# Kernel optimization log

Hardware: AMD Instinct MI355X
Metric: run time of the kernel (lower is better)

## Reference

```python
import jax, jax.numpy as jnp
import numpy as np

B, S = 1, 2048
HIDDEN = 2560
NH, NKV, HD = 32, 8, 128
GS = 128  # awq group size
ROPE_THETA = 1000000.0


def dequant_q4(qweight, scales, qzeros):
    """Unpack int4 AWQ weights -> dense [K, N] float weight.
    qweight: [K//8, N] int32, 8 nibbles packed along the input (K) dim.
    scales/qzeros: [K//GS, N]. w = (nibble - zero) * scale.
    """
    K8, N = qweight.shape
    shifts = jnp.arange(8, dtype=jnp.int32) * 4
    nib = (qweight[:, None, :] >> shifts[None, :, None]) & 0xF  # [K//8, 8, N]
    w = nib.reshape(K8 * 8, N).astype(scales.dtype)             # [K, N]
    z = jnp.repeat(qzeros.astype(scales.dtype), GS, axis=0)     # [K, N]
    s = jnp.repeat(scales, GS, axis=0)                          # [K, N]
    return (w - z) * s


def linear_q4(x, qw, sc, qz, bias=None):
    w = dequant_q4(qw, sc, qz)                     # [K, N]
    y = jnp.einsum('bsk,kn->bsn', x, w)
    return y + bias if bias is not None else y


def rotate_half(x):
    x1, x2 = jnp.split(x, 2, axis=-1)
    return jnp.concatenate([-x2, x1], axis=-1)


def apply_rope(q, k, cos, sin):
    # cos/sin: [B, S, HD] -> broadcast over heads at dim 2
    c = cos[:, :, None, :]
    s = sin[:, :, None, :]
    return q * c + rotate_half(q) * s, k * c + rotate_half(k) * s


def setup_inputs() -> dict:
    key = jax.random.key(0)
    ks = jax.random.split(key, 12)

    x = jax.random.normal(ks[0], (B, S, HIDDEN), dtype=jnp.float32)

    # genuine rotary embedding tables
    inv_freq = 1.0 / (ROPE_THETA ** (np.arange(0, HD, 2, dtype=np.float32) / HD))
    t = np.arange(S, dtype=np.float32)
    freqs = np.outer(t, inv_freq)                      # [S, HD/2]
    emb = np.concatenate([freqs, freqs], axis=-1)      # [S, HD]
    cos = jnp.asarray(np.cos(emb)[None], dtype=jnp.float32)  # [1, S, HD]
    sin = jnp.asarray(np.sin(emb)[None], dtype=jnp.float32)

    def mk_proj(kq, ksc, kz, K, N, group=GS):
        qw = jax.random.randint(kq, (K // 8, N), 0, 2**31 - 1, dtype=jnp.int32)
        sc = jax.random.normal(ksc, (K // group, N), dtype=jnp.float32) * 0.01
        qz = jax.random.randint(kz, (K // group, N), 0, 16, dtype=jnp.int32)
        return qw, sc, qz

    q_qweight, q_scales, q_qzeros = mk_proj(ks[1], ks[2], ks[3], HIDDEN, NH * HD)
    k_qweight, k_scales, k_qzeros = mk_proj(ks[4], ks[5], ks[6], HIDDEN, NKV * HD)
    v_qweight, v_scales, v_qzeros = mk_proj(ks[7], ks[8], ks[9], HIDDEN, NKV * HD)
    o_qweight, o_scales, o_qzeros = mk_proj(ks[10], ks[11], jax.random.fold_in(key, 99), NH * HD, HIDDEN)

    kb = jax.random.split(jax.random.fold_in(key, 7), 3)
    q_bias = jax.random.normal(kb[0], (NH * HD,), dtype=jnp.float32) * 0.02
    k_bias = jax.random.normal(kb[1], (NKV * HD,), dtype=jnp.float32) * 0.02
    v_bias = jax.random.normal(kb[2], (NKV * HD,), dtype=jnp.float32) * 0.02

    return dict(x=x, cos=cos, sin=sin,
                q_scales=q_scales, q_bias=q_bias,
                k_scales=k_scales, k_bias=k_bias,
                v_scales=v_scales, v_bias=v_bias,
                o_scales=o_scales,
                q_qweight=q_qweight, q_qzeros=q_qzeros,
                k_qweight=k_qweight, k_qzeros=k_qzeros,
                v_qweight=v_qweight, v_qzeros=v_qzeros,
                o_qweight=o_qweight, o_qzeros=o_qzeros)


def reference(x, cos, sin,
              q_scales, q_bias, k_scales, k_bias, v_scales, v_bias, o_scales,
              q_qweight, q_qzeros, k_qweight, k_qzeros,
              v_qweight, v_qzeros, o_qweight, o_qzeros):
    b, s, _ = x.shape
    xq = linear_q4(x, q_qweight, q_scales, q_qzeros, q_bias).reshape(b, s, NH, HD)
    xk = linear_q4(x, k_qweight, k_scales, k_qzeros, k_bias).reshape(b, s, NKV, HD)
    xv = linear_q4(x, v_qweight, v_scales, v_qzeros, v_bias).reshape(b, s, NKV, HD)

    xq, xk = apply_rope(xq, xk, cos, sin)

    # GQA: repeat KV heads to match query heads (prefill, start_pos=0)
    rep = NH // NKV
    xk = jnp.repeat(xk, rep, axis=2)   # [b, s, NH, HD]
    xv = jnp.repeat(xv, rep, axis=2)

    scale = 1.0 / jnp.sqrt(jnp.asarray(HD, dtype=xq.dtype))
    scores = jnp.einsum('bqhd,bkhd->bhqk', xq, xk) * scale  # [b, NH, s, s]
    causal = jnp.tril(jnp.ones((s, s), dtype=bool))
    scores = jnp.where(causal[None, None], scores, jnp.finfo(scores.dtype).min)
    attn = jax.nn.softmax(scores, axis=-1)
    out = jnp.einsum('bhqk,bkhd->bqhd', attn, xv).reshape(b, s, NH * HD)

    return linear_q4(out, o_qweight, o_scales, o_qzeros)  # [b, s, HIDDEN]
```

## Files before the change

kernel.cpp:

```cpp
#include <hip/hip_runtime.h>
#include <hip/hip_bf16.h>
#include <cstdint>

#define S_LEN 2048
#define HIDDEN 2560
#define NH 32
#define NKV 8
#define HD 128
#define GS 128

typedef __attribute__((ext_vector_type(8))) _Float16 half8v;
typedef __attribute__((ext_vector_type(2))) _Float16 half2v;
typedef __attribute__((ext_vector_type(4))) float f32x4;
typedef unsigned int uint;
typedef unsigned short ushort;

__device__ inline ushort f2h(float f) {
    _Float16 h = (_Float16)f;
    return __builtin_bit_cast(ushort, h);
}
__device__ inline float h2f(ushort u) {
    return (float)__builtin_bit_cast(_Float16, u);
}
__device__ inline uint pk2(ushort a, ushort b) { return (uint)a | ((uint)b << 16); }

__device__ __attribute__((always_inline)) inline void gl_lds16(const void* g, void* l) {
    __builtin_amdgcn_global_load_lds(
        (const __attribute__((address_space(1))) unsigned int*)g,
        (__attribute__((address_space(3))) unsigned int*)l, 16, 0, 0);
}

__global__ __launch_bounds__(320) void xcvt_kernel(
    const float* __restrict__ X, ushort* __restrict__ Xf)
{
    const int row = blockIdx.x;
    const int t   = threadIdx.x;
    const size_t base = (size_t)row * HIDDEN + t * 8;
    float4 a = *(const float4*)&X[base];
    float4 b = *(const float4*)&X[base + 4];
    uint4 hw = {pk2(f2h(a.x), f2h(a.y)), pk2(f2h(a.z), f2h(a.w)),
                pk2(f2h(b.x), f2h(b.y)), pk2(f2h(b.z), f2h(b.w))};
    *(uint4*)&Xf[base] = hw;
}

__global__ __launch_bounds__(512) void qkv5_kernel(
    const ushort* __restrict__ Xf,
    const int* __restrict__ q_qw, const float* __restrict__ q_sc,
    const int* __restrict__ q_qz, const float* __restrict__ q_b,
    const int* __restrict__ k_qw, const float* __restrict__ k_sc,
    const int* __restrict__ k_qz, const float* __restrict__ k_b,
    const int* __restrict__ v_qw, const float* __restrict__ v_sc,
    const int* __restrict__ v_qz, const float* __restrict__ v_b,
    const float* __restrict__ cosb, const float* __restrict__ sinb,
    ushort* __restrict__ Qf, ushort* __restrict__ Kf,
    ushort* __restrict__ Vrm)
{
    __shared__ __align__(16) char LDSB[65536];
    ushort* A0 = (ushort*)(LDSB);
    ushort* A1 = (ushort*)(LDSB + 16384);
    ushort* Bt = (ushort*)(LDSB + 32768);

    const int t  = threadIdx.x;
    const int w  = t >> 6;
    const int l  = t & 63;
    const int lg = l >> 4;
    const int lr = l & 15;
    const int wr = w >> 2;
    const int wc = w & 3;
    const int K  = HIDDEN;

    const int bid = blockIdx.x;
    const int swz = (bid & 7) * 48 + (bid >> 3);
    const int nblk = swz % 24;
    const int m0   = (swz / 24) * 128;

    int region, nbase, Nw;
    const int* QW; const float* SC; const int* QZ; const float* BI;
    if (nblk < 16)      { region = 0; nbase = nblk * 256;        Nw = NH * HD;
                          QW = q_qw; SC = q_sc; QZ = q_qz; BI = q_b; }
    else if (nblk < 20) { region = 1; nbase = (nblk - 16) * 256; Nw = NKV * HD;
                          QW = k_qw; SC = k_sc; QZ = k_qz; BI = k_b; }
    else                { region = 2; nbase = (nblk - 20) * 256; Nw = NKV * HD;
                          QW = v_qw; SC = v_sc; QZ = v_qz; BI = v_b; }

    const int am0 = t >> 3, ac0 = t & 7;
    const size_t aoff0 = (size_t)(m0 + am0) * K + (size_t)((ac0 ^ (am0 & 7)) * 8);
    const size_t aoff1 = aoff0 + (size_t)64 * K;
    const int ldsA0 = w * 1024;
    const int ldsA1 = 8192 + w * 1024;
    const int bn  = t & 255;
    const int bk0 = (t >> 8) * 4;
    int bwoff[4];
#pragma unroll
    for (int j = 0; j < 4; ++j)
        bwoff[j] = (bn * 128 + (bk0 + j) * 16) ^ ((bn & 7) << 4);

    int ncm[4];
#pragma unroll
    for (int nf = 0; nf < 4; ++nf)
        ncm[nf] = (wc >> 1) * 128 + ((nf & 2) ? 64 : 0) + (wc & 1) * 32 + (nf & 1) * 16 + lr;

    const int xorA = (lr & 7) << 4;
    int aroff[4][2], broff[4][2];
#pragma unroll
    for (int mf = 0; mf < 4; ++mf)
#pragma unroll
        for (int ks = 0; ks < 2; ++ks)
            aroff[mf][ks] = (((wr * 64 + mf * 16 + lr) * 128) + lg * 16 + ks * 64) ^ xorA;
#pragma unroll
    for (int nf = 0; nf < 4; ++nf)
#pragma unroll
        for (int ks = 0; ks < 2; ++ks)
            broff[nf][ks] = ((ncm[nf] * 128) + lg * 16 + ks * 64) ^ xorA;

    f32x4 macc[4][4];
#pragma unroll
    for (int mf = 0; mf < 4; ++mf)
#pragma unroll
        for (int nf = 0; nf < 4; ++nf) macc[mf][nf] = f32x4{0.f, 0.f, 0.f, 0.f};
    uint qr[4];
    float scf, zf;

#define QKV_QW(tile) { int g8 = (tile) * 8; int gg = (tile) >> 1; \
    _Pragma("unroll") \
    for (int j = 0; j < 4; ++j) \
        qr[j] = (uint)QW[(size_t)(g8 + bk0 + j) * Nw + nbase + bn]; \
    scf = SC[(size_t)gg * Nw + nbase + bn]; \
    zf  = (float)QZ[(size_t)gg * Nw + nbase + bn]; }

#define QKV_STAGE_A(AH, k0) { \
    gl_lds16(Xf + (k0) + aoff0, (char*)(AH) + ldsA0); \
    gl_lds16(Xf + (k0) + aoff1, (char*)(AH) + ldsA1); }

#define QKV_BWRITE(BT) { \
    ushort sch = f2h(scf); \
    float schf = h2f(sch); \
    ushort msc = f2h(-128.0f * schf);    \
    ushort nzs = f2h(-(zf * schf)); \
    half2v S2 = {__builtin_bit_cast(_Float16, sch), __builtin_bit_cast(_Float16, sch)}; \
    half2v M2 = {__builtin_bit_cast(_Float16, msc), __builtin_bit_cast(_Float16, msc)}; \
    half2v Z2 = {__builtin_bit_cast(_Float16, nzs), __builtin_bit_cast(_Float16, nzs)}; \
    _Pragma("unroll") \
    for (int j = 0; j < 4; ++j) { \
        uint q = qr[j]; \
        uint b0 = q & 0xFFu, b1 = (q >> 8) & 0xFFu, b2 = (q >> 16) & 0xFFu, b3 = q >> 24; \
        uint e0 = 0x58005800u | ((b0 & 0xFu) << 3) | ((b0 & 0xF0u) << 15); \
        uint e1 = 0x58005800u | ((b1 & 0xFu) << 3) | ((b1 & 0xF0u) << 15); \
        uint e2 = 0x58005800u | ((b2 & 0xFu) << 3) | ((b2 & 0xF0u) << 15); \
        uint e3 = 0x58005800u | ((b3 & 0xFu) << 3) | ((b3 & 0xF0u) << 15); \
        half2v w0 = __builtin_bit_cast(half2v, e0) * S2 + M2; w0 = w0 + Z2; \
        half2v w1 = __builtin_bit_cast(half2v, e1) * S2 + M2; w1 = w1 + Z2; \
        half2v w2 = __builtin_bit_cast(half2v, e2) * S2 + M2; w2 = w2 + Z2; \
        half2v w3 = __builtin_bit_cast(half2v, e3) * S2 + M2; w3 = w3 + Z2; \
        uint4 dw = {__builtin_bit_cast(uint, w0), __builtin_bit_cast(uint, w1), \
                    __builtin_bit_cast(uint, w2), __builtin_bit_cast(uint, w3)}; \
        *(uint4*)((char*)(BT) + bwoff[j]) = dw; \
    } }

#define QKV_COMPUTE(AH, BT) { \
    _Pragma("unroll") \
    for (int ks = 0; ks < 2; ++ks) { \
        half8v av[4], bv[4]; \
        _Pragma("unroll") \
        for (int mf = 0; mf < 4; ++mf) \
            av[mf] = *(const half8v*)((const char*)(AH) + aroff[mf][ks]); \
        _Pragma("unroll") \
        for (int nf = 0; nf < 4; ++nf) \
            bv[nf] = *(const half8v*)((const char*)(BT) + broff[nf][ks]); \
        _Pragma("unroll") \
        for (int mf = 0; mf < 4; ++mf) \
            _Pragma("unroll") \
            for (int nf = 0; nf < 4; ++nf) \
                macc[mf][nf] = __builtin_amdgcn_mfma_f32_16x16x32_f16(av[mf], bv[nf], macc[mf][nf], 0, 0, 0); \
    } }

    QKV_QW(0);
    QKV_BWRITE(Bt);
    QKV_STAGE_A(A0, 0);
    QKV_QW(1);
    __syncthreads();

    for (int g = 0; g < 20; ++g) {
        QKV_COMPUTE(A0, Bt);
        __syncthreads();
        QKV_BWRITE(Bt);
        QKV_STAGE_A(A1, (2 * g + 1) * 64);
        if (g < 19) QKV_QW(2 * g + 2);
        __syncthreads();
        QKV_COMPUTE(A1, Bt);
        __syncthreads();
        if (g < 19) {
            QKV_BWRITE(Bt);
            QKV_STAGE_A(A0, (2 * g + 2) * 64);
            QKV_QW(2 * g + 3);
        }
        __syncthreads();
    }

#pragma unroll
    for (int nf = 0; nf < 4; ++nf) {
        float bv = BI[nbase + ncm[nf]];
#pragma unroll
        for (int mf = 0; mf < 4; ++mf)
#pragma unroll
            for (int r = 0; r < 4; ++r) macc[mf][nf][r] += bv;
    }

    if (region == 2) {
#pragma unroll
        for (int mf = 0; mf < 4; ++mf)
#pragma unroll
            for (int r = 0; r < 4; ++r) {
                int row = m0 + wr * 64 + mf * 16 + lg * 4 + r;
#pragma unroll
                for (int nf = 0; nf < 4; ++nf)
                    Vrm[(size_t)row * (NKV * HD) + nbase + ncm[nf]] = f2h(macc[mf][nf][r]);
            }
    } else {
        ushort* OF = (region == 0) ? Qf : Kf;
        const int No = (region == 0) ? NH * HD : NKV * HD;
        const float osc = (region == 0) ? 0.08838834764831845f : 1.0f;
        const int colb = nbase + (wc >> 1) * 128;
#pragma unroll
        for (int mf = 0; mf < 4; ++mf)
#pragma unroll
            for (int r = 0; r < 4; ++r) {
                int row = m0 + wr * 64 + mf * 16 + lg * 4 + r;
                const float* cb = &cosb[(size_t)row * HD];
                const float* sb = &sinb[(size_t)row * HD];
#pragma unroll
                for (int nf = 0; nf < 2; ++nf) {
                    int d = (wc & 1) * 32 + nf * 16 + lr;
                    float a = macc[mf][nf][r];
                    float b = macc[mf][nf + 2][r];
                    float o1 = (a * cb[d]      - b * sb[d])      * osc;
                    float o2 = (b * cb[d + 64] + a * sb[d + 64]) * osc;
                    OF[(size_t)row * No + colb + d]      = f2h(o1);
                    OF[(size_t)row * No + colb + d + 64] = f2h(o2);
                }
            }
    }
#undef QKV_QW
#undef QKV_STAGE_A
#undef QKV_BWRITE
#undef QKV_COMPUTE
}

__global__ __launch_bounds__(256) void vtrans_kernel(
    const ushort* __restrict__ Vrm, ushort* __restrict__ VfT)
{
    __shared__ ushort Ts[64][65];
    const int s0 = blockIdx.x * 64;
    const int n0 = blockIdx.y * 64;
    const int t  = threadIdx.x;
    {
        int r = t >> 2, c0 = (t & 3) * 16;
        uint4 v0 = *(const uint4*)&Vrm[(size_t)(s0 + r) * (NKV * HD) + n0 + c0];
        uint4 v1 = *(const uint4*)&Vrm[(size_t)(s0 + r) * (NKV * HD) + n0 + c0 + 8];
        const ushort* pv = (const ushort*)&v0;
#pragma unroll
        for (int j = 0; j < 8; ++j) Ts[r][c0 + j] = pv[j];
        pv = (const ushort*)&v1;
#pragma unroll
        for (int j = 0; j < 8; ++j) Ts[r][c0 + 8 + j] = pv[j];
    }
    __syncthreads();
    {
        int rn = t >> 2, cs0 = (t & 3) * 16;
        ushort ob[16];
#pragma unroll
        for (int j = 0; j < 16; ++j) ob[j] = Ts[cs0 + j][rn];
        ushort* dst = &VfT[(size_t)(n0 + rn) * S_LEN + s0 + cs0];
        *(uint4*)dst = ((uint4*)ob)[0];
        *(uint4*)(dst + 8) = ((uint4*)ob)[1];
    }
}

__global__ __launch_bounds__(512) void oproj4_kernel(
    const ushort* __restrict__ Xb, const int* __restrict__ QW,
    const float* __restrict__ SC, const int* __restrict__ QZ,
    float* __restrict__ Y)
{
    __shared__ __align__(16) char LDSB[65536];
    ushort* A0  = (ushort*)(LDSB);
    ushort* A1  = (ushort*)(LDSB + 16384);
    ushort* Bt0 = (ushort*)(LDSB + 32768);
    ushort* Bt1 = (ushort*)(LDSB + 49152);

    const int t  = threadIdx.x;
    const int w  = t >> 6;
    const int l  = t & 63;
    const int lg = l >> 4;
    const int lr = l & 15;
    const int wr = w >> 2;
    const int wc = w & 3;
    const int K  = NH * HD;
    const int N  = HIDDEN;

    const int bid = blockIdx.x;
    const int swz = (bid & 7) * 40 + (bid >> 3);
    const int n0  = (swz % 20) * 128;
    const int m0  = (swz / 20) * 128;

    const int am0 = t >> 3, ac0 = t & 7;
    const size_t aoff0 = (size_t)(m0 + am0) * K + (size_t)((ac0 ^ (am0 & 7)) * 8);
    const size_t aoff1 = aoff0 + (size_t)64 * K;
    const int ldsA0 = w * 1024;
    const int ldsA1 = 8192 + w * 1024;
    const int bn  = t & 127;
    const int bk0 = (t >> 7) * 2;
    int bwoff[2];
#pragma unroll
    for (int j = 0; j < 2; ++j)
        bwoff[j] = (bn * 128 + (bk0 + j) * 16) ^ ((bn & 7) << 4);

    const int xorA = (lr & 7) << 4;
    int aroff[4][2], broff[2][2];
#pragma unroll
    for (int mf = 0; mf < 4; ++mf)
#pragma unroll
        for (int ks = 0; ks < 2; ++ks)
            aroff[mf][ks] = (((wr * 64 + mf * 16 + lr) * 128) + lg * 16 + ks * 64) ^ xorA;
#pragma unroll
    for (int nf = 0; nf < 2; ++nf)
#pragma unroll
        for (int ks = 0; ks < 2; ++ks)
            broff[nf][ks] = (((wc * 32 + nf * 16 + lr) * 128) + lg * 16 + ks * 64) ^ xorA;

    f32x4 macc[4][2];
#pragma unroll
    for (int mf = 0; mf < 4; ++mf)
#pragma unroll
        for (int nf = 0; nf < 2; ++nf) macc[mf][nf] = f32x4{0.f, 0.f, 0.f, 0.f};
    uint qr[2];
    float scf, zf;

#define OP_QW(tile) { int g8 = (tile) * 8; int gg = (tile) >> 1; \
    _Pragma("unroll") \
    for (int j = 0; j < 2; ++j) \
        qr[j] = (uint)QW[(size_t)(g8 + bk0 + j) * N + n0 + bn]; \
    scf = SC[(size_t)gg * N + n0 + bn]; \
    zf  = (float)QZ[(size_t)gg * N + n0 + bn]; }

#define OP_STAGE_A(AH, k0) { \
    gl_lds16(Xb + (k0) + aoff0, (char*)(AH) + ldsA0); \
    gl_lds16(Xb + (k0) + aoff1, (char*)(AH) + ldsA1); }

#define OP_BWRITE(BT) { \
    ushort sch = f2h(scf); \
    float schf = h2f(sch); \
    ushort msc = f2h(-128.0f * schf); \
    ushort nzs = f2h(-(zf * schf)); \
    half2v S2 = {__builtin_bit_cast(_Float16, sch), __builtin_bit_cast(_Float16, sch)}; \
    half2v M2 = {__builtin_bit_cast(_Float16, msc), __builtin_bit_cast(_Float16, msc)}; \
    half2v Z2 = {__builtin_bit_cast(_Float16, nzs), __builtin_bit_cast(_Float16, nzs)}; \
    _Pragma("unroll") \
    for (int j = 0; j < 2; ++j) { \
        uint q = qr[j]; \
        uint b0 = q & 0xFFu, b1 = (q >> 8) & 0xFFu, b2 = (q >> 16) & 0xFFu, b3 = q >> 24; \
        uint e0 = 0x58005800u | ((b0 & 0xFu) << 3) | ((b0 & 0xF0u) << 15); \
        uint e1 = 0x58005800u | ((b1 & 0xFu) << 3) | ((b1 & 0xF0u) << 15); \
        uint e2 = 0x58005800u | ((b2 & 0xFu) << 3) | ((b2 & 0xF0u) << 15); \
        uint e3 = 0x58005800u | ((b3 & 0xFu) << 3) | ((b3 & 0xF0u) << 15); \
        half2v w0 = __builtin_bit_cast(half2v, e0) * S2 + M2; w0 = w0 + Z2; \
        half2v w1 = __builtin_bit_cast(half2v, e1) * S2 + M2; w1 = w1 + Z2; \
        half2v w2 = __builtin_bit_cast(half2v, e2) * S2 + M2; w2 = w2 + Z2; \
        half2v w3 = __builtin_bit_cast(half2v, e3) * S2 + M2; w3 = w3 + Z2; \
        uint4 dw = {__builtin_bit_cast(uint, w0), __builtin_bit_cast(uint, w1), \
                    __builtin_bit_cast(uint, w2), __builtin_bit_cast(uint, w3)}; \
        *(uint4*)((char*)(BT) + bwoff[j]) = dw; \
    } }

#define OP_COMPUTE(AH, BT) { \
    _Pragma("unroll") \
    for (int ks = 0; ks < 2; ++ks) { \
        half8v av[4], bv[2]; \
        _Pragma("unroll") \
        for (int mf = 0; mf < 4; ++mf) \
            av[mf] = *(const half8v*)((const char*)(AH) + aroff[mf][ks]); \
        _Pragma("unroll") \
        for (int nf = 0; nf < 2; ++nf) \
            bv[nf] = *(const half8v*)((const char*)(BT) + broff[nf][ks]); \
        _Pragma("unroll") \
        for (int mf = 0; mf < 4; ++mf) \
            _Pragma("unroll") \
            for (int nf = 0; nf < 2; ++nf) \
                macc[mf][nf] = __builtin_amdgcn_mfma_f32_16x16x32_f16(av[mf], bv[nf], macc[mf][nf], 0, 0, 0); \
    } }

    OP_QW(0);
    OP_STAGE_A(A0, 0);
    OP_BWRITE(Bt0);
    __syncthreads();

    for (int g = 0; g < 32; ++g) {
        const int t1 = 2 * g + 1;
        OP_QW(t1);
        OP_STAGE_A(A1, t1 * 64);
        OP_COMPUTE(A0, Bt0);
        OP_BWRITE(Bt1);
        __syncthreads();
        if (g < 31) {
            const int t2 = 2 * g + 2;
            OP_QW(t2);
            OP_STAGE_A(A0, t2 * 64);
        }
        OP_COMPUTE(A1, Bt1);
        if (g < 31) OP_BWRITE(Bt0);
        __syncthreads();
    }

#pragma unroll
    for (int mf = 0; mf < 4; ++mf)
#pragma unroll
        for (int r = 0; r < 4; ++r) {
            int row = m0 + wr * 64 + mf * 16 + lg * 4 + r;
#pragma unroll
            for (int nf = 0; nf < 2; ++nf)
                Y[(size_t)row * N + n0 + wc * 32 + nf * 16 + lr] = macc[mf][nf][r];
        }
#undef OP_QW
#undef OP_STAGE_A
#undef OP_BWRITE
#undef OP_COMPUTE
}

__global__ __launch_bounds__(256) void attn_mfma_kernel(
    const ushort* __restrict__ Qh,
    const ushort* __restrict__ Kh,
    const ushort* __restrict__ Vt,
    ushort* __restrict__ AO)
{
    __shared__ ushort KsF[32 * 128];
    __shared__ ushort Vs[128 * 32];
    __shared__ __align__(16) char PsB[4 * 1280];

    const int h  = blockIdx.x;
    const int qb = gridDim.y - 1 - blockIdx.y;
    const int s0 = qb * 64;
    const int t  = threadIdx.x;
    const int w  = t >> 6;
    const int l  = t & 63;
    const int lg = l >> 4;
    const int lr = l & 15;
    const int kvh = h >> 2;
    const int qw = s0 + w * 16;
    const int q  = qw + lr;

    half8v qf[4];
#pragma unroll
    for (int d = 0; d < 4; ++d) {
        size_t off = (size_t)q * (NH * HD) + h * HD + d * 32 + lg * 8;
        qf[d] = *(const half8v*)&Qh[off];
    }

    f32x4 o[8];
#pragma unroll
    for (int i = 0; i < 8; ++i) o[i] = f32x4{0.f, 0.f, 0.f, 0.f};
    float m = -1e30f, lsum = 0.f;
    char* pw = PsB + w * 1280;

    const int ntiles = qb * 2 + 2;
    for (int kt = 0; kt < ntiles; ++kt) {
        const int k0 = kt * 32;
#pragma unroll
        for (int i = 0; i < 2; ++i) {
            int slot = w * 128 + i * 64 + l;
            int mr = slot >> 4, c = slot & 15;
            size_t goff = (size_t)(k0 + mr) * (NKV * HD) + kvh * HD + ((c ^ (mr & 7)) * 8);
            gl_lds16(Kh + goff, (char*)KsF + (w * 128 + i * 64) * 16);
        }
#pragma unroll
        for (int i = 0; i < 2; ++i) {
            int slot = w * 128 + i * 64 + l;
            int dim = slot >> 2, c = slot & 3;
            size_t goff = (size_t)(kvh * HD + dim) * S_LEN + k0 + ((c ^ (dim & 3)) * 8);
            gl_lds16(Vt + goff, (char*)Vs + (w * 128 + i * 64) * 16);
        }
        __syncthreads();

        if (k0 <= qw + 15) {
            f32x4 s[2];
            s[0] = f32x4{0.f, 0.f, 0.f, 0.f};
            s[1] = f32x4{0.f, 0.f, 0.f, 0.f};
#pragma unroll
            for (int d = 0; d < 4; ++d) {
#pragma unroll
                for (int nt2 = 0; nt2 < 2; ++nt2) {
                    int row = nt2 * 16 + lr;
                    int off = row * 256 + ((d * 64 + lg * 16) ^ ((row & 7) << 4));
                    half8v kf = *(const half8v*)((char*)KsF + off);
                    s[nt2] = __builtin_amdgcn_mfma_f32_16x16x32_f16(kf, qf[d], s[nt2], 0, 0, 0);
                }
            }
            float sv[8];
#pragma unroll
            for (int nt2 = 0; nt2 < 2; ++nt2)
#pragma unroll
                for (int r = 0; r < 4; ++r) {
                    int kv = k0 + nt2 * 16 + lg * 4 + r;
                    sv[nt2 * 4 + r] = (kv <= q) ? s[nt2][r] : -1e30f;
                }
            float mx = sv[0];
#pragma unroll
            for (int j = 1; j < 8; ++j) mx = fmaxf(mx, sv[j]);
            mx = fmaxf(mx, __shfl_xor(mx, 16));
            mx = fmaxf(mx, __shfl_xor(mx, 32));
            float mnew = fmaxf(m, mx);
            float resc = __expf(m - mnew);
            m = mnew;
            float p[8], ps = 0.f;
#pragma unroll
            for (int j = 0; j < 8; ++j) { p[j] = __expf(sv[j] - mnew); ps += p[j]; }
            ps += __shfl_xor(ps, 16);
            ps += __shfl_xor(ps, 32);
            lsum = lsum * resc + ps;
#pragma unroll
            for (int dt = 0; dt < 8; ++dt)
#pragma unroll
                for (int r = 0; r < 4; ++r) o[dt][r] *= resc;
            uint2 w0 = {pk2(f2h(p[0]), f2h(p[1])), pk2(f2h(p[2]), f2h(p[3]))};
            uint2 w1 = {pk2(f2h(p[4]), f2h(p[5])), pk2(f2h(p[6]), f2h(p[7]))};
            *(uint2*)(pw + lr * 80 + lg * 8)      = w0;
            *(uint2*)(pw + lr * 80 + 32 + lg * 8) = w1;
            asm volatile("s_waitcnt lgkmcnt(0)" ::: "memory");
            half8v pf = *(const half8v*)(pw + lr * 80 + lg * 16);
#pragma unroll
            for (int dt = 0; dt < 8; ++dt) {
                int dim = dt * 16 + lr;
                half8v vf = *(const half8v*)((char*)Vs + dim * 64 + ((lg * 16) ^ ((dim & 3) << 4)));
                o[dt] = __builtin_amdgcn_mfma_f32_16x16x32_f16(vf, pf, o[dt], 0, 0, 0);
            }
        }
        __syncthreads();
    }

    float inv = 1.f / lsum;
    ushort* dst = &AO[(size_t)q * (NH * HD) + h * HD];
#pragma unroll
    for (int dt = 0; dt < 8; ++dt) {
        uint2 ov = {pk2(f2h(o[dt][0] * inv), f2h(o[dt][1] * inv)),
                    pk2(f2h(o[dt][2] * inv), f2h(o[dt][3] * inv))};
        *(uint2*)(dst + dt * 16 + lg * 4) = ov;
    }
}

extern "C" void kernel_launch(void* const* d_in, const int* in_sizes, int n_in,
                              void* d_out, int out_size, void* d_ws, size_t ws_size,
                              hipStream_t stream)
{
    const float* x    = (const float*)d_in[0];
    const float* cosb = (const float*)d_in[1];
    const float* sinb = (const float*)d_in[2];
    const float* q_sc = (const float*)d_in[3];
    const float* q_b  = (const float*)d_in[4];
    const float* k_sc = (const float*)d_in[5];
    const float* k_b  = (const float*)d_in[6];
    const float* v_sc = (const float*)d_in[7];
    const float* v_b  = (const float*)d_in[8];
    const float* o_sc = (const float*)d_in[9];
    const int* q_qw   = (const int*)d_in[10];
    const int* q_qz   = (const int*)d_in[11];
    const int* k_qw   = (const int*)d_in[12];
    const int* k_qz   = (const int*)d_in[13];
    const int* v_qw   = (const int*)d_in[14];
    const int* v_qz   = (const int*)d_in[15];
    const int* o_qw   = (const int*)d_in[16];
    const int* o_qz   = (const int*)d_in[17];
    float* out = (float*)d_out;

    char* ws = (char*)d_ws;
    ushort* Xf   = (ushort*)ws;
    ushort* AOf  = (ushort*)ws;
    ushort* Qf   = (ushort*)(ws + (size_t)16 * 1024 * 1024);
    ushort* Kf   = (ushort*)(ws + (size_t)32 * 1024 * 1024);
    ushort* Vrm  = (ushort*)(ws + (size_t)36 * 1024 * 1024);
    ushort* VfT  = (ushort*)(ws + (size_t)40 * 1024 * 1024);

    xcvt_kernel<<<S_LEN, 320, 0, stream>>>(x, Xf);

    qkv5_kernel<<<384, 512, 0, stream>>>(
        Xf,
        q_qw, q_sc, q_qz, q_b,
        k_qw, k_sc, k_qz, k_b,
        v_qw, v_sc, v_qz, v_b,
        cosb, sinb, Qf, Kf, Vrm);

    vtrans_kernel<<<dim3(S_LEN / 64, (NKV * HD) / 64), 256, 0, stream>>>(Vrm, VfT);

    attn_mfma_kernel<<<dim3(NH, S_LEN / 64), 256, 0, stream>>>(Qf, Kf, VfT, AOf);

    oproj4_kernel<<<320, 512, 0, stream>>>(
        AOf, o_qw, o_sc, o_qz, out);
}
```

Measured before the change: 286.7 us.

## Shrink QKV and O-proj GEMM blocks to 256 threads with 128x128 tiles

The fused QKV projection kernel now uses 256-thread blocks with 128x128 output tiles, doubling the grid to 768 blocks. The output projection kernel moves to 256 threads, with each wave computing a 64x64 sub-tile. It also uses a single B buffer with extra barriers in place of the double-buffered B tile. The goal is more blocks per CU, through smaller LDS (48KB) and more grid parallelism, at the cost of more per-wave register accumulators and more synchronisation in the O-proj pipeline.

New measurement: 287.2 us. Within noise of the previous version (+0.2%).

```diff
diff --git a/kernel.cpp b/kernel.cpp
--- a/kernel.cpp
+++ b/kernel.cpp
@@ -43,7 +43,7 @@
     *(uint4*)&Xf[base] = hw;
 }
 
-__global__ __launch_bounds__(512) void qkv5_kernel(
+__global__ __launch_bounds__(256) void qkv6_kernel(
     const ushort* __restrict__ Xf,
     const int* __restrict__ q_qw, const float* __restrict__ q_sc,
     const int* __restrict__ q_qz, const float* __restrict__ q_b,
@@ -55,7 +55,7 @@
     ushort* __restrict__ Qf, ushort* __restrict__ Kf,
     ushort* __restrict__ Vrm)
 {
-    __shared__ __align__(16) char LDSB[65536];
+    __shared__ __align__(16) char LDSB[49152];
     ushort* A0 = (ushort*)(LDSB);
     ushort* A1 = (ushort*)(LDSB + 16384);
     ushort* Bt = (ushort*)(LDSB + 32768);
@@ -65,31 +65,34 @@
     const int l  = t & 63;
     const int lg = l >> 4;
     const int lr = l & 15;
-    const int wr = w >> 2;
-    const int wc = w & 3;
+    const int wr = w >> 1;
+    const int wc = w & 1;
     const int K  = HIDDEN;
 
     const int bid = blockIdx.x;
-    const int swz = (bid & 7) * 48 + (bid >> 3);
-    const int nblk = swz % 24;
-    const int m0   = (swz / 24) * 128;
+    const int swz = (bid & 7) * 96 + (bid >> 3);
+    const int nblk = swz % 48;
+    const int m0   = (swz / 48) * 128;
 
     int region, nbase, Nw;
     const int* QW; const float* SC; const int* QZ; const float* BI;
-    if (nblk < 16)      { region = 0; nbase = nblk * 256;        Nw = NH * HD;
+    if (nblk < 32)      { region = 0; nbase = nblk * 128;        Nw = NH * HD;
                           QW = q_qw; SC = q_sc; QZ = q_qz; BI = q_b; }
-    else if (nblk < 20) { region = 1; nbase = (nblk - 16) * 256; Nw = NKV * HD;
+    else if (nblk < 40) { region = 1; nbase = (nblk - 32) * 128; Nw = NKV * HD;
                           QW = k_qw; SC = k_sc; QZ = k_qz; BI = k_b; }
-    else                { region = 2; nbase = (nblk - 20) * 256; Nw = NKV * HD;
+    else                { region = 2; nbase = (nblk - 40) * 128; Nw = NKV * HD;
                           QW = v_qw; SC = v_sc; QZ = v_qz; BI = v_b; }
 
-    const int am0 = t >> 3, ac0 = t & 7;
-    const size_t aoff0 = (size_t)(m0 + am0) * K + (size_t)((ac0 ^ (am0 & 7)) * 8);
-    const size_t aoff1 = aoff0 + (size_t)64 * K;
-    const int ldsA0 = w * 1024;
-    const int ldsA1 = 8192 + w * 1024;
-    const int bn  = t & 255;
-    const int bk0 = (t >> 8) * 4;
+    const int ldsAw = w * 1024;
+    size_t aoff[4];
+#pragma unroll
+    for (int i = 0; i < 4; ++i) {
+        int slot = i * 256 + t;
+        int am = slot >> 3, ac = slot & 7;
+        aoff[i] = (size_t)(m0 + am) * K + (size_t)((ac ^ (am & 7)) * 8);
+    }
+    const int bn  = t & 127;
+    const int bk0 = (t >> 7) * 4;
     int bwoff[4];
 #pragma unroll
     for (int j = 0; j < 4; ++j)
@@ -98,7 +101,7 @@
     int ncm[4];
 #pragma unroll
     for (int nf = 0; nf < 4; ++nf)
-        ncm[nf] = (wc >> 1) * 128 + ((nf & 2) ? 64 : 0) + (wc & 1) * 32 + (nf & 1) * 16 + lr;
+        ncm[nf] = wc * 32 + (nf & 1) * 16 + lr + ((nf & 2) ? 64 : 0);
 
     const int xorA = (lr & 7) << 4;
     int aroff[4][2], broff[4][2];
@@ -129,8 +132,10 @@
     zf  = (float)QZ[(size_t)gg * Nw + nbase + bn]; }
 
 #define QKV_STAGE_A(AH, k0) { \
-    gl_lds16(Xf + (k0) + aoff0, (char*)(AH) + ldsA0); \
-    gl_lds16(Xf + (k0) + aoff1, (char*)(AH) + ldsA1); }
+    gl_lds16(Xf + (k0) + aoff[0], (char*)(AH) + ldsAw); \
+    gl_lds16(Xf + (k0) + aoff[1], (char*)(AH) + 4096 + ldsAw); \
+    gl_lds16(Xf + (k0) + aoff[2], (char*)(AH) + 8192 + ldsAw); \
+    gl_lds16(Xf + (k0) + aoff[3], (char*)(AH) + 12288 + ldsAw); }
 
 #define QKV_BWRITE(BT) { \
     ushort sch = f2h(scf); \
@@ -220,7 +225,6 @@
         ushort* OF = (region == 0) ? Qf : Kf;
         const int No = (region == 0) ? NH * HD : NKV * HD;
         const float osc = (region == 0) ? 0.08838834764831845f : 1.0f;
-        const int colb = nbase + (wc >> 1) * 128;
 #pragma unroll
         for (int mf = 0; mf < 4; ++mf)
 #pragma unroll
@@ -230,13 +234,13 @@
                 const float* sb = &sinb[(size_t)row * HD];
 #pragma unroll
                 for (int nf = 0; nf < 2; ++nf) {
-                    int d = (wc & 1) * 32 + nf * 16 + lr;
+                    int d = wc * 32 + nf * 16 + lr;
                     float a = macc[mf][nf][r];
                     float b = macc[mf][nf + 2][r];
                     float o1 = (a * cb[d]      - b * sb[d])      * osc;
                     float o2 = (b * cb[d + 64] + a * sb[d + 64]) * osc;
-                    OF[(size_t)row * No + colb + d]      = f2h(o1);
-                    OF[(size_t)row * No + colb + d + 64] = f2h(o2);
+                    OF[(size_t)row * No + nbase + d]      = f2h(o1);
+                    OF[(size_t)row * No + nbase + d + 64] = f2h(o2);
                 }
             }
     }
@@ -276,24 +280,23 @@
     }
 }
 
-__global__ __launch_bounds__(512) void oproj4_kernel(
+__global__ __launch_bounds__(256) void oproj5_kernel(
     const ushort* __restrict__ Xb, const int* __restrict__ QW,
     const float* __restrict__ SC, const int* __restrict__ QZ,
     float* __restrict__ Y)
 {
-    __shared__ __align__(16) char LDSB[65536];
-    ushort* A0  = (ushort*)(LDSB);
-    ushort* A1  = (ushort*)(LDSB + 16384);
-    ushort* Bt0 = (ushort*)(LDSB + 32768);
-    ushort* Bt1 = (ushort*)(LDSB + 49152);
+    __shared__ __align__(16) char LDSB[49152];
+    ushort* A0 = (ushort*)(LDSB);
+    ushort* A1 = (ushort*)(LDSB + 16384);
+    ushort* Bt = (ushort*)(LDSB + 32768);
 
     const int t  = threadIdx.x;
     const int w  = t >> 6;
     const int l  = t & 63;
     const int lg = l >> 4;
     const int lr = l & 15;
-    const int wr = w >> 2;
-    const int wc = w & 3;
+    const int wr = w >> 1;
+    const int wc = w & 1;
     const int K  = NH * HD;
     const int N  = HIDDEN;
 
@@ -302,49 +305,54 @@
     const int n0  = (swz % 20) * 128;
     const int m0  = (swz / 20) * 128;
 
-    const int am0 = t >> 3, ac0 = t & 7;
-    const size_t aoff0 = (size_t)(m0 + am0) * K + (size_t)((ac0 ^ (am0 & 7)) * 8);
-    const size_t aoff1 = aoff0 + (size_t)64 * K;
-    const int ldsA0 = w * 1024;
-    const int ldsA1 = 8192 + w * 1024;
+    const int ldsAw = w * 1024;
+    size_t aoff[4];
+#pragma unroll
+    for (int i = 0; i < 4; ++i) {
+        int slot = i * 256 + t;
+        int am = slot >> 3, ac = slot & 7;
+        aoff[i] = (size_t)(m0 + am) * K + (size_t)((ac ^ (am & 7)) * 8);
+    }
     const int bn  = t & 127;
-    const int bk0 = (t >> 7) * 2;
-    int bwoff[2];
-#pragma unroll
-    for (int j = 0; j < 2; ++j)
+    const int bk0 = (t >> 7) * 4;
+    int bwoff[4];
+#pragma unroll
+    for (int j = 0; j < 4; ++j)
         bwoff[j] = (bn * 128 + (bk0 + j) * 16) ^ ((bn & 7) << 4);
 
     const int xorA = (lr & 7) << 4;
-    int aroff[4][2], broff[2][2];
+    int aroff[4][2], broff[4][2];
 #pragma unroll
     for (int mf = 0; mf < 4; ++mf)
 #pragma unroll
         for (int ks = 0; ks < 2; ++ks)
             aroff[mf][ks] = (((wr * 64 + mf * 16 + lr) * 128) + lg * 16 + ks * 64) ^ xorA;
 #pragma unroll
-    for (int nf = 0; nf < 2; ++nf)
+    for (int nf = 0; nf < 4; ++nf)
 #pragma unroll
         for (int ks = 0; ks < 2; ++ks)
-            broff[nf][ks] = (((wc * 32 + nf * 16 + lr) * 128) + lg * 16 + ks * 64) ^ xorA;
-
-    f32x4 macc[4][2];
+            broff[nf][ks] = (((wc * 64 + nf * 16 + lr) * 128) + lg * 16 + ks * 64) ^ xorA;
+
+    f32x4 macc[4][4];
 #pragma unroll
     for (int mf = 0; mf < 4; ++mf)
 #pragma unroll
-        for (int nf = 0; nf < 2; ++nf) macc[mf][nf] = f32x4{0.f, 0.f, 0.f, 0.f};
-    uint qr[2];
+        for (int nf = 0; nf < 4; ++nf) macc[mf][nf] = f32x4{0.f, 0.f, 0.f, 0.f};
+    uint qr[4];
     float scf, zf;
 
 #define OP_QW(tile) { int g8 = (tile) * 8; int gg = (tile) >> 1; \
     _Pragma("unroll") \
-    for (int j = 0; j < 2; ++j) \
+    for (int j = 0; j < 4; ++j) \
         qr[j] = (uint)QW[(size_t)(g8 + bk0 + j) * N + n0 + bn]; \
     scf = SC[(size_t)gg * N + n0 + bn]; \
     zf  = (float)QZ[(size_t)gg * N + n0 + bn]; }
 
 #define OP_STAGE_A(AH, k0) { \
-    gl_lds16(Xb + (k0) + aoff0, (char*)(AH) + ldsA0); \
-    gl_lds16(Xb + (k0) + aoff1, (char*)(AH) + ldsA1); }
+    gl_lds16(Xb + (k0) + aoff[0], (char*)(AH) + ldsAw); \
+    gl_lds16(Xb + (k0) + aoff[1], (char*)(AH) + 4096 + ldsAw); \
+    gl_lds16(Xb + (k0) + aoff[2], (char*)(AH) + 8192 + ldsAw); \
+    gl_lds16(Xb + (k0) + aoff[3], (char*)(AH) + 12288 + ldsAw); }
 
 #define OP_BWRITE(BT) { \
     ushort sch = f2h(scf); \
@@ -355,7 +363,7 @@
     half2v M2 = {__builtin_bit_cast(_Float16, msc), __builtin_bit_cast(_Float16, msc)}; \
     half2v Z2 = {__builtin_bit_cast(_Float16, nzs), __builtin_bit_cast(_Float16, nzs)}; \
     _Pragma("unroll") \
-    for (int j = 0; j < 2; ++j) { \
+    for (int j = 0; j < 4; ++j) { \
         uint q = qr[j]; \
         uint b0 = q & 0xFFu, b1 = (q >> 8) & 0xFFu, b2 = (q >> 16) & 0xFFu, b3 = q >> 24; \
         uint e0 = 0x58005800u | ((b0 & 0xFu) << 3) | ((b0 & 0xF0u) << 15); \
@@ -374,39 +382,40 @@
 #define OP_COMPUTE(AH, BT) { \
     _Pragma("unroll") \
     for (int ks = 0; ks < 2; ++ks) { \
-        half8v av[4], bv[2]; \
+        half8v av[4], bv[4]; \
         _Pragma("unroll") \
         for (int mf = 0; mf < 4; ++mf) \
             av[mf] = *(const half8v*)((const char*)(AH) + aroff[mf][ks]); \
         _Pragma("unroll") \
-        for (int nf = 0; nf < 2; ++nf) \
+        for (int nf = 0; nf < 4; ++nf) \
             bv[nf] = *(const half8v*)((const char*)(BT) + broff[nf][ks]); \
         _Pragma("unroll") \
         for (int mf = 0; mf < 4; ++mf) \
             _Pragma("unroll") \
-            for (int nf = 0; nf < 2; ++nf) \
+            for (int nf = 0; nf < 4; ++nf) \
                 macc[mf][nf] = __builtin_amdgcn_mfma_f32_16x16x32_f16(av[mf], bv[nf], macc[mf][nf], 0, 0, 0); \
     } }
 
     OP_QW(0);
+    OP_BWRITE(Bt);
     OP_STAGE_A(A0, 0);
-    OP_BWRITE(Bt0);
+    OP_QW(1);
     __syncthreads();
 
     for (int g = 0; g < 32; ++g) {
-        const int t1 = 2 * g + 1;
-        OP_QW(t1);
-        OP_STAGE_A(A1, t1 * 64);
-        OP_COMPUTE(A0, Bt0);
-        OP_BWRITE(Bt1);
+        OP_COMPUTE(A0, Bt);
+        __syncthreads();
+        OP_BWRITE(Bt);
+        OP_STAGE_A(A1, (2 * g + 1) * 64);
+        if (g < 31) OP_QW(2 * g + 2);
+        __syncthreads();
+        OP_COMPUTE(A1, Bt);
         __syncthreads();
         if (g < 31) {
-            const int t2 = 2 * g + 2;
-            OP_QW(t2);
-            OP_STAGE_A(A0, t2 * 64);
+            OP_BWRITE(Bt);
+            OP_STAGE_A(A0, (2 * g + 2) * 64);
+            OP_QW(2 * g + 3);
         }
-        OP_COMPUTE(A1, Bt1);
-        if (g < 31) OP_BWRITE(Bt0);
         __syncthreads();
     }
 
@@ -416,8 +425,8 @@
         for (int r = 0; r < 4; ++r) {
             int row = m0 + wr * 64 + mf * 16 + lg * 4 + r;
 #pragma unroll
-            for (int nf = 0; nf < 2; ++nf)
-                Y[(size_t)row * N + n0 + wc * 32 + nf * 16 + lr] = macc[mf][nf][r];
+            for (int nf = 0; nf < 4; ++nf)
+                Y[(size_t)row * N + n0 + wc * 64 + nf * 16 + lr] = macc[mf][nf][r];
         }
 #undef OP_QW
 #undef OP_STAGE_A
@@ -579,7 +588,7 @@
 
     xcvt_kernel<<<S_LEN, 320, 0, stream>>>(x, Xf);
 
-    qkv5_kernel<<<384, 512, 0, stream>>>(
+    qkv6_kernel<<<768, 256, 0, stream>>>(
         Xf,
         q_qw, q_sc, q_qz, q_b,
         k_qw, k_sc, k_qz, k_b,
@@ -590,6 +599,6 @@
 
     attn_mfma_kernel<<<dim3(NH, S_LEN / 64), 256, 0, stream>>>(Qf, Kf, VfT, AOf);
 
-    oproj4_kernel<<<320, 512, 0, stream>>>(
+    oproj5_kernel<<<320, 256, 0, stream>>>(
         AOf, o_qw, o_sc, o_qz, out);
 }
```
